# Kernel optimization log

Hardware: AMD Instinct MI355X
Metric: run time of the kernel (lower is better)

## Reference

```python
import jax, jax.numpy as jnp
import numpy as np
import math

B, T, C = 2, 2048, 1024
N_HEADS = 16  # config.head_size in the original (actually number of heads)
HEAD_DIM = C // N_HEADS


def setup_inputs() -> dict:
    key = jax.random.key(0)
    k1, k2, k3 = jax.random.split(key, 3)
    s = 1.0 / math.sqrt(C)
    return {
        "x": jax.random.normal(k1, (B, T, C), dtype=jnp.float32),
        "W_attn": jax.random.normal(k2, (C, 3 * C), dtype=jnp.float32) * s,
        "b_attn": jnp.zeros((3 * C,), dtype=jnp.float32),
        "W_proj": jax.random.normal(k3, (C, C), dtype=jnp.float32) * s,
        "b_proj": jnp.zeros((C,), dtype=jnp.float32),
    }


def reference(x, W_attn, b_attn, W_proj, b_proj):
    Bsz, Tlen, Cdim = x.shape
    qkv = x @ W_attn + b_attn                      # [B,T,3C]
    q, k, v = jnp.split(qkv, 3, axis=-1)
    # [B,T,C] -> [B,H,T,D]
    def to_heads(t):
        return t.reshape(Bsz, Tlen, N_HEADS, HEAD_DIM).transpose(0, 2, 1, 3)
    q, k, v = to_heads(q), to_heads(k), to_heads(v)
    # NOTE: original multiplies by sqrt(head_dim) (faithful to source, not 1/sqrt)
    scale = jnp.asarray(math.sqrt(HEAD_DIM), dtype=x.dtype)
    att = jnp.einsum("bhqd,bhkd->bhqk", q, k) * scale
    causal = jnp.tril(jnp.ones((Tlen, Tlen), dtype=bool))
    att = jnp.where(causal[None, None, :, :], att, jnp.asarray(-jnp.inf, x.dtype))
    att = jax.nn.softmax(att, axis=-1)
    # dropout layers are identity in eval mode
    y = jnp.einsum("bhqk,bhkd->bhqd", att, v)
    y = y.transpose(0, 2, 1, 3).reshape(Bsz, Tlen, Cdim)
    return y @ W_proj + b_proj
```

## Files before the change

### kernel.cpp

```cpp
#include <hip/hip_runtime.h>
#include <hip/hip_bf16.h>


#define B_  2
#define T_  2048
#define C_  1024
#define H_  16
#define D_  64
#define M_  (B_ * T_)
#define N3_ (3 * C_)

typedef __attribute__((ext_vector_type(8))) short s16x8;
typedef __attribute__((ext_vector_type(4))) short s16x4;
typedef __attribute__((ext_vector_type(4))) float f32x4;

typedef const __attribute__((address_space(1))) unsigned int gu32_t;
typedef __attribute__((address_space(3))) unsigned int lu32_t;

__device__ __forceinline__ void gload_lds16(const short* g, short* l) {
    __builtin_amdgcn_global_load_lds((gu32_t*)g, (lu32_t*)l, 16, 0, 0);
}

__device__ __forceinline__ float b2f(unsigned short u) {
    return __uint_as_float(((unsigned)u) << 16);
}
__device__ __forceinline__ unsigned short f2b(float f) {
    unsigned u = __float_as_uint(f);
    return (unsigned short)((u + 0x7FFFu + ((u >> 16) & 1u)) >> 16);
}

__global__ __launch_bounds__(256) void cvt_split(
    const float* __restrict__ in, short* __restrict__ oh, short* __restrict__ ol, int n)
{
    int i = (blockIdx.x * 256 + threadIdx.x) * 8;
    if (i >= n) return;
    float4 a = *(const float4*)&in[i];
    float4 b = *(const float4*)&in[i + 4];
    float v[8] = {a.x, a.y, a.z, a.w, b.x, b.y, b.z, b.w};
    s16x8 h, l;
    #pragma unroll
    for (int j = 0; j < 8; j++) {
        unsigned short hb = f2b(v[j]);
        h[j] = (short)hb;
        l[j] = (short)f2b(v[j] - b2f(hb));
    }
    *(s16x8*)&oh[i] = h;
    *(s16x8*)&ol[i] = l;
}

__global__ __launch_bounds__(256) void cvtT_split(
    const float* __restrict__ in, short* __restrict__ oh, short* __restrict__ ol,
    int R, int Cn)
{
    __shared__ short th[64][80];
    __shared__ short tl[64][80];
    const int tid = threadIdx.x;
    const int k0 = blockIdx.y * 64;
    const int n0 = blockIdx.x * 64;
    {
        int rl = tid >> 4, cl = (tid & 15) * 4;
        #pragma unroll
        for (int i = 0; i < 4; i++) {
            int kr = rl + i * 16;
            float4 v4 = *(const float4*)&in[(size_t)(k0 + kr) * Cn + n0 + cl];
            float v[4] = {v4.x, v4.y, v4.z, v4.w};
            #pragma unroll
            for (int j = 0; j < 4; j++) {
                unsigned short hb = f2b(v[j]);
                th[cl + j][kr] = (short)hb;
                tl[cl + j][kr] = (short)f2b(v[j] - b2f(hb));
            }
        }
    }
    __syncthreads();
    {
        int ro = tid >> 2, co = (tid & 3) * 16;
        *(s16x8*)&oh[(size_t)(n0 + ro) * R + k0 + co]     = *(s16x8*)&th[ro][co];
        *(s16x8*)&oh[(size_t)(n0 + ro) * R + k0 + co + 8] = *(s16x8*)&th[ro][co + 8];
        *(s16x8*)&ol[(size_t)(n0 + ro) * R + k0 + co]     = *(s16x8*)&tl[ro][co];
        *(s16x8*)&ol[(size_t)(n0 + ro) * R + k0 + co + 8] = *(s16x8*)&tl[ro][co + 8];
    }
}

__global__ __launch_bounds__(256) void cvtT_bf16(
    const float* __restrict__ in, short* __restrict__ out, int R, int Cn)
{
    __shared__ short t[64][80];
    const int tid = threadIdx.x;
    const int k0 = blockIdx.y * 64;
    const int n0 = blockIdx.x * 64;
    {
        int rl = tid >> 4, cl = (tid & 15) * 4;
        #pragma unroll
        for (int i = 0; i < 4; i++) {
            int kr = rl + i * 16;
            float4 v = *(const float4*)&in[(size_t)(k0 + kr) * Cn + n0 + cl];
            t[cl + 0][kr] = (short)f2b(v.x);
            t[cl + 1][kr] = (short)f2b(v.y);
            t[cl + 2][kr] = (short)f2b(v.z);
            t[cl + 3][kr] = (short)f2b(v.w);
        }
    }
    __syncthreads();
    {
        int ro = tid >> 2, co = (tid & 3) * 16;
        *(s16x8*)&out[(size_t)(n0 + ro) * R + k0 + co]     = *(s16x8*)&t[ro][co];
        *(s16x8*)&out[(size_t)(n0 + ro) * R + k0 + co + 8] = *(s16x8*)&t[ro][co + 8];
    }
}

__global__ __launch_bounds__(256) void qkv_qk(
    const short* __restrict__ Ah, const short* __restrict__ Al,
    const short* __restrict__ BTh, const short* __restrict__ BTl,
    const float* __restrict__ bias,
    short* __restrict__ Qh, short* __restrict__ Ql,
    short* __restrict__ Kh, short* __restrict__ Kl)
{
    __shared__ short Ash[128 * 32], Asl[128 * 32];
    __shared__ short Bsh[128 * 32], Bsl[128 * 32];

    const int tid  = threadIdx.x;
    const int wave = tid >> 6, lane = tid & 63;
    const int wm = wave >> 1, wn = wave & 1;
    const int lm = lane & 15, lq = lane >> 4;
    const int m0 = blockIdx.y * 128, n0 = blockIdx.x * 128;
    const int gr = (lane >> 2);
    const int gc = (lane & 3) * 8;

    f32x4 acc[4][4] = {};

    for (int k0 = 0; k0 < C_; k0 += 32) {
        __syncthreads();
        #pragma unroll
        for (int j = 0; j < 2; j++) {
            int s = wave * 2 + j;
            int row = s * 16 + gr;
            size_t ga = (size_t)(m0 + row) * C_ + k0 + gc;
            size_t gb = (size_t)(n0 + row) * C_ + k0 + gc;
            gload_lds16(&Ah[ga],  &Ash[s * 512]);
            gload_lds16(&Al[ga],  &Asl[s * 512]);
            gload_lds16(&BTh[gb], &Bsh[s * 512]);
            gload_lds16(&BTl[gb], &Bsl[s * 512]);
        }
        __syncthreads();

        s16x8 ah[4], al[4], bh[4], bl[4];
        #pragma unroll
        for (int mi = 0; mi < 4; mi++) {
            int r = wm * 64 + mi * 16 + lm;
            ah[mi] = *(const s16x8*)&Ash[r * 32 + lq * 8];
            al[mi] = *(const s16x8*)&Asl[r * 32 + lq * 8];
        }
        #pragma unroll
        for (int nj = 0; nj < 4; nj++) {
            int r = wn * 64 + nj * 16 + lm;
            bh[nj] = *(const s16x8*)&Bsh[r * 32 + lq * 8];
            bl[nj] = *(const s16x8*)&Bsl[r * 32 + lq * 8];
        }
        #pragma unroll
        for (int mi = 0; mi < 4; mi++)
            #pragma unroll
            for (int nj = 0; nj < 4; nj++) {
                acc[mi][nj] = __builtin_amdgcn_mfma_f32_16x16x32_bf16(
                    ah[mi], bh[nj], acc[mi][nj], 0, 0, 0);
                acc[mi][nj] = __builtin_amdgcn_mfma_f32_16x16x32_bf16(
                    ah[mi], bl[nj], acc[mi][nj], 0, 0, 0);
                acc[mi][nj] = __builtin_amdgcn_mfma_f32_16x16x32_bf16(
                    al[mi], bh[nj], acc[mi][nj], 0, 0, 0);
            }
    }

    #pragma unroll
    for (int nj = 0; nj < 4; nj++) {
        int n = n0 + wn * 64 + nj * 16 + lm;
        float bv = bias[n];
        int isK = n >> 10;
        int c = n & (C_ - 1);
        int h = c >> 6, d = c & (D_ - 1);
        short* dh = isK ? Kh : Qh;
        short* dl = isK ? Kl : Ql;
        #pragma unroll
        for (int mi = 0; mi < 4; mi++) {
            #pragma unroll
            for (int r = 0; r < 4; r++) {
                int m  = m0 + wm * 64 + mi * 16 + lq * 4 + r;
                int bb = m >> 11, t = m & (T_ - 1);
                float v = acc[mi][nj][r] + bv;
                size_t idx = (((size_t)bb * H_ + h) * T_ + t) * D_ + d;
                unsigned short hb = f2b(v);
                dh[idx] = (short)hb;
                dl[idx] = (short)f2b(v - b2f(hb));
            }
        }
    }
}

__global__ __launch_bounds__(256) void qkv_v(
    const short* __restrict__ Ah, const short* __restrict__ BTh,
    const float* __restrict__ bias, short* __restrict__ VT)
{
    __shared__ short Ash[128 * 32];
    __shared__ short Bsh[128 * 32];

    const int tid  = threadIdx.x;
    const int wave = tid >> 6, lane = tid & 63;
    const int wm = wave >> 1, wn = wave & 1;
    const int lm = lane & 15, lq = lane >> 4;
    const int m0 = blockIdx.y * 128, n0 = blockIdx.x * 128;
    const int gr = (lane >> 2);
    const int gc = (lane & 3) * 8;

    f32x4 acc[4][4] = {};

    for (int k0 = 0; k0 < C_; k0 += 32) {
        __syncthreads();
        #pragma unroll
        for (int j = 0; j < 2; j++) {
            int s = wave * 2 + j;
            int row = s * 16 + gr;
            gload_lds16(&Ah[(size_t)(m0 + row) * C_ + k0 + gc],  &Ash[s * 512]);
            gload_lds16(&BTh[(size_t)(n0 + row) * C_ + k0 + gc], &Bsh[s * 512]);
        }
        __syncthreads();

        s16x8 af[4], bfr[4];
        #pragma unroll
        for (int mi = 0; mi < 4; mi++)
            af[mi] = *(const s16x8*)&Ash[(wm * 64 + mi * 16 + lm) * 32 + lq * 8];
        #pragma unroll
        for (int nj = 0; nj < 4; nj++)
            bfr[nj] = *(const s16x8*)&Bsh[(wn * 64 + nj * 16 + lm) * 32 + lq * 8];
        #pragma unroll
        for (int mi = 0; mi < 4; mi++)
            #pragma unroll
            for (int nj = 0; nj < 4; nj++)
                acc[mi][nj] = __builtin_amdgcn_mfma_f32_16x16x32_bf16(
                    af[mi], bfr[nj], acc[mi][nj], 0, 0, 0);
    }

    #pragma unroll
    for (int nj = 0; nj < 4; nj++) {
        int n = n0 + wn * 64 + nj * 16 + lm;
        float bv = bias[n];
        int h = n >> 6, d = n & (D_ - 1);
        #pragma unroll
        for (int mi = 0; mi < 4; mi++) {
            #pragma unroll
            for (int r = 0; r < 4; r++) {
                int m  = m0 + wm * 64 + mi * 16 + lq * 4 + r;
                int bb = m >> 11, t = m & (T_ - 1);
                VT[(((size_t)bb * H_ + h) * D_ + d) * T_ + t] =
                    (short)f2b(acc[mi][nj][r] + bv);
            }
        }
    }
}

__global__ __launch_bounds__(256) void proj_mfma(
    const short* __restrict__ A, const short* __restrict__ BT,
    const float* __restrict__ bias, float* __restrict__ out)
{
    __shared__ short Ash[128 * 32];
    __shared__ short Bsh[128 * 32];

    const int tid  = threadIdx.x;
    const int wave = tid >> 6, lane = tid & 63;
    const int wm = wave >> 1, wn = wave & 1;
    const int lm = lane & 15, lq = lane >> 4;
    const int m0 = blockIdx.y * 128, n0 = blockIdx.x * 128;
    const int gr = (lane >> 2);
    const int gc = (lane & 3) * 8;

    f32x4 acc[4][4] = {};

    for (int k0 = 0; k0 < C_; k0 += 32) {
        __syncthreads();
        #pragma unroll
        for (int j = 0; j < 2; j++) {
            int s = wave * 2 + j;
            int row = s * 16 + gr;
            gload_lds16(&A[(size_t)(m0 + row) * C_ + k0 + gc],  &Ash[s * 512]);
            gload_lds16(&BT[(size_t)(n0 + row) * C_ + k0 + gc], &Bsh[s * 512]);
        }
        __syncthreads();

        s16x8 af[4], bfr[4];
        #pragma unroll
        for (int mi = 0; mi < 4; mi++)
            af[mi] = *(const s16x8*)&Ash[(wm * 64 + mi * 16 + lm) * 32 + lq * 8];
        #pragma unroll
        for (int nj = 0; nj < 4; nj++)
            bfr[nj] = *(const s16x8*)&Bsh[(wn * 64 + nj * 16 + lm) * 32 + lq * 8];
        #pragma unroll
        for (int mi = 0; mi < 4; mi++)
            #pragma unroll
            for (int nj = 0; nj < 4; nj++)
                acc[mi][nj] = __builtin_amdgcn_mfma_f32_16x16x32_bf16(
                    af[mi], bfr[nj], acc[mi][nj], 0, 0, 0);
    }

    #pragma unroll
    for (int nj = 0; nj < 4; nj++) {
        int n = n0 + wn * 64 + nj * 16 + lm;
        float bv = bias[n];
        #pragma unroll
        for (int mi = 0; mi < 4; mi++) {
            #pragma unroll
            for (int r = 0; r < 4; r++) {
                int m = m0 + wm * 64 + mi * 16 + lq * 4 + r;
                out[(size_t)m * C_ + n] = acc[mi][nj][r] + bv;
            }
        }
    }
}

__global__ __launch_bounds__(256) void attn_mfma(
    const short* __restrict__ Qh, const short* __restrict__ Ql,
    const short* __restrict__ Kh, const short* __restrict__ Kl,
    const short* __restrict__ VT, short* __restrict__ Yb)
{
    __shared__ short Qsh[64][72], Qsl[64][72];
    __shared__ short Ksh[64][72], Ksl[64][72];
    __shared__ short Vt [64][72];
    __shared__ short Ps [4][16][72];

    const int tid  = threadIdx.x;
    const int wave = tid >> 6, lane = tid & 63;
    const int lm   = lane & 15, quad = lane >> 4;
    const int bh   = blockIdx.y;
    const int b    = bh >> 4, h = bh & (H_ - 1);
    const size_t base = (size_t)bh * T_ * D_;
    const size_t vbase = (size_t)bh * D_ * T_;

    for (int half = 0; half < 2; half++) {
        const int qt = (half == 0) ? blockIdx.x : 31 - blockIdx.x;
        const int q0 = qt * 64;

        __syncthreads();
        #pragma unroll
        for (int i = 0; i < 2; i++) {
            int c = i * 256 + tid;
            int row = c >> 3, ch = (c & 7) * 8;
            size_t g = base + (size_t)(q0 + row) * D_ + ch;
            *(s16x8*)&Qsh[row][ch] = *(const s16x8*)&Qh[g];
            *(s16x8*)&Qsl[row][ch] = *(const s16x8*)&Ql[g];
        }
        __syncthreads();

        s16x8 bqh[2], bql[2];
        #pragma unroll
        for (int kc = 0; kc < 2; kc++) {
            bqh[kc] = *(const s16x8*)&Qsh[wave * 16 + lm][kc * 32 + quad * 8];
            bql[kc] = *(const s16x8*)&Qsl[wave * 16 + lm][kc * 32 + quad * 8];
        }

        float mrow = -INFINITY, lrow = 0.f;
        f32x4 O[4] = {};

        for (int kt = 0; kt <= qt; kt++) {
            __syncthreads();
            #pragma unroll
            for (int i = 0; i < 2; i++) {
                int c = i * 256 + tid;
                int row = c >> 3, ch = (c & 7) * 8;
                size_t g = base + (size_t)(kt * 64 + row) * D_ + ch;
                *(s16x8*)&Ksh[row][ch] = *(const s16x8*)&Kh[g];
                *(s16x8*)&Ksl[row][ch] = *(const s16x8*)&Kl[g];
            }
            #pragma unroll
            for (int i = 0; i < 2; i++) {
                int c = i * 256 + tid;
                int d = c >> 3, ch = (c & 7) * 8;
                *(s16x8*)&Vt[d][ch] =
                    *(const s16x8*)&VT[vbase + (size_t)d * T_ + kt * 64 + ch];
            }
            __syncthreads();

            f32x4 S[4] = {};
            #pragma unroll
            for (int t = 0; t < 4; t++) {
                #pragma unroll
                for (int kc = 0; kc < 2; kc++) {
                    s16x8 kh8 = *(const s16x8*)&Ksh[t * 16 + lm][kc * 32 + quad * 8];
                    s16x8 kl8 = *(const s16x8*)&Ksl[t * 16 + lm][kc * 32 + quad * 8];
                    S[t] = __builtin_amdgcn_mfma_f32_16x16x32_bf16(kh8, bqh[kc], S[t], 0, 0, 0);
                    S[t] = __builtin_amdgcn_mfma_f32_16x16x32_bf16(kl8, bqh[kc], S[t], 0, 0, 0);
                    S[t] = __builtin_amdgcn_mfma_f32_16x16x32_bf16(kh8, bql[kc], S[t], 0, 0, 0);
                }
            }

            const int qg = wave * 16 + lm;
            #pragma unroll
            for (int t = 0; t < 4; t++)
                #pragma unroll
                for (int r = 0; r < 4; r++) {
                    float v = S[t][r] * 8.0f;
                    if (kt == qt && (t * 16 + quad * 4 + r) > qg) v = -INFINITY;
                    S[t][r] = v;
                }

            float rm = -INFINITY;
            #pragma unroll
            for (int t = 0; t < 4; t++)
                #pragma unroll
                for (int r = 0; r < 4; r++) rm = fmaxf(rm, S[t][r]);
            rm = fmaxf(rm, __shfl_xor(rm, 16, 64));
            rm = fmaxf(rm, __shfl_xor(rm, 32, 64));
            float mnew  = fmaxf(mrow, rm);
            float alpha = __expf(mrow - mnew);
            mrow = mnew;
            float rs = 0.f;
            #pragma unroll
            for (int t = 0; t < 4; t++)
                #pragma unroll
                for (int r = 0; r < 4; r++) {
                    S[t][r] = __expf(S[t][r] - mnew);
                    rs += S[t][r];
                }
            rs += __shfl_xor(rs, 16, 64);
            rs += __shfl_xor(rs, 32, 64);
            lrow = lrow * alpha + rs;

            float al[4];
            #pragma unroll
            for (int r = 0; r < 4; r++) al[r] = __shfl(alpha, quad * 4 + r, 64);
            #pragma unroll
            for (int t = 0; t < 4; t++)
                #pragma unroll
                for (int r = 0; r < 4; r++) O[t][r] *= al[r];

            #pragma unroll
            for (int t = 0; t < 4; t++) {
                s16x4 p;
                #pragma unroll
                for (int r = 0; r < 4; r++) p[r] = (short)f2b(S[t][r]);
                *(s16x4*)&Ps[wave][lm][t * 16 + quad * 4] = p;
            }

            s16x8 ap[2];
            #pragma unroll
            for (int kc = 0; kc < 2; kc++)
                ap[kc] = *(const s16x8*)&Ps[wave][lm][kc * 32 + quad * 8];
            #pragma unroll
            for (int t = 0; t < 4; t++) {
                #pragma unroll
                for (int kc = 0; kc < 2; kc++) {
                    s16x8 bv = *(const s16x8*)&Vt[t * 16 + lm][kc * 32 + quad * 8];
                    O[t] = __builtin_amdgcn_mfma_f32_16x16x32_bf16(ap[kc], bv, O[t], 0, 0, 0);
                }
            }
        }

        float li[4];
        #pragma unroll
        for (int r = 0; r < 4; r++)
            li[r] = 1.0f / __shfl(lrow, quad * 4 + r, 64);
        #pragma unroll
        for (int t = 0; t < 4; t++)
            #pragma unroll
            for (int r = 0; r < 4; r++) {
                int q = q0 + wave * 16 + quad * 4 + r;
                int d = t * 16 + lm;
                Yb[((size_t)b * T_ + q) * C_ + h * D_ + d] =
                    (short)f2b(O[t][r] * li[r]);
            }
    }
}

extern "C" void kernel_launch(void* const* d_in, const int* in_sizes, int n_in,
                              void* d_out, int out_size, void* d_ws, size_t ws_size,
                              hipStream_t stream)
{
    const float* x      = (const float*)d_in[0];
    const float* W_attn = (const float*)d_in[1];
    const float* b_attn = (const float*)d_in[2];
    const float* W_proj = (const float*)d_in[3];
    const float* b_proj = (const float*)d_in[4];
    float* out = (float*)d_out;

    char* ws = (char*)d_ws;
    const size_t MB = 1024 * 1024;
    short* Qh   = (short*)(ws);
    short* Ql   = (short*)(ws +  8 * MB);
    short* Kh   = (short*)(ws + 16 * MB);
    short* Kl   = (short*)(ws + 24 * MB);
    short* xh   = (short*)(ws + 32 * MB);
    short* xl   = (short*)(ws + 40 * MB);
    short* WaTh = (short*)(ws + 48 * MB);
    short* WaTl = (short*)(ws + 54 * MB);
    short* WpT  = (short*)(ws + 60 * MB);
    short* VT   = (short*)(ws + 40 * MB);
    short* Yb   = (short*)(ws + 32 * MB);

    cvt_split <<<dim3(M_ * C_ / 2048), 256, 0, stream>>>(x, xh, xl, M_ * C_);
    cvtT_split<<<dim3(N3_ / 64, C_ / 64), 256, 0, stream>>>(W_attn, WaTh, WaTl, C_, N3_);
    cvtT_bf16 <<<dim3(C_ / 64, C_ / 64), 256, 0, stream>>>(W_proj, WpT, C_, C_);

    qkv_qk <<<dim3(16, 32), 256, 0, stream>>>(xh, xl, WaTh, WaTl, b_attn,
                                              Qh, Ql, Kh, Kl);
    qkv_v  <<<dim3(8, 32), 256, 0, stream>>>(xh, WaTh + (size_t)2048 * C_,
                                             b_attn + 2048, VT);
    attn_mfma<<<dim3(16, 32), 256, 0, stream>>>(Qh, Ql, Kh, Kl, VT, Yb);
    proj_mfma<<<dim3(8, 32), 256, 0, stream>>>(Yb, WpT, b_proj, out);
}
```

Before: 265.3 us.

## Prefetch K/V tiles into registers, fold Q scale, remap blocks per XCD

The attention kernel now loads the next K/V tile into registers while the current tile is being computed, which overlaps global latency with MFMA work. The sqrt(D) scale is folded into Q at the QKV projection epilogue, and the causal mask is applied only on the diagonal tile. The grid is flattened and remapped so that blocks sharing a head land on the same XCD, which should improve L2 reuse. P is converted to bf16 by truncation instead of rounding, and scaling Q before the hi/lo split changes numerics slightly; together these may cost some accuracy and add register pressure.

```diff
diff --git a/kernel.cpp b/kernel.cpp
--- a/kernel.cpp
+++ b/kernel.cpp
@@ -179,13 +179,14 @@
         int h = c >> 6, d = c & (D_ - 1);
         short* dh = isK ? Kh : Qh;
         short* dl = isK ? Kl : Ql;
+        float scale = isK ? 1.0f : 8.0f;
         #pragma unroll
         for (int mi = 0; mi < 4; mi++) {
             #pragma unroll
             for (int r = 0; r < 4; r++) {
                 int m  = m0 + wm * 64 + mi * 16 + lq * 4 + r;
                 int bb = m >> 11, t = m & (T_ - 1);
-                float v = acc[mi][nj][r] + bv;
+                float v = (acc[mi][nj][r] + bv) * scale;
                 size_t idx = (((size_t)bb * H_ + h) * T_ + t) * D_ + d;
                 unsigned short hb = f2b(v);
                 dh[idx] = (short)hb;
@@ -327,23 +328,30 @@
     const int tid  = threadIdx.x;
     const int wave = tid >> 6, lane = tid & 63;
     const int lm   = lane & 15, quad = lane >> 4;
-    const int bh   = blockIdx.y;
-    const int b    = bh >> 4, h = bh & (H_ - 1);
-    const size_t base = (size_t)bh * T_ * D_;
+
+    const int bid = blockIdx.x;
+    const int xcd = bid & 7, s = bid >> 3;
+    const int bh  = xcd * 4 + (s >> 4);
+    const int qx  = s & 15;
+    const int b   = bh >> 4, h = bh & (H_ - 1);
+    const size_t base  = (size_t)bh * T_ * D_;
     const size_t vbase = (size_t)bh * D_ * T_;
 
+    s16x8 pkh[2], pkl[2], pvt[2];
+    const int src = tid >> 3;
+    const int sch = (tid & 7) * 8;
+
     for (int half = 0; half < 2; half++) {
-        const int qt = (half == 0) ? blockIdx.x : 31 - blockIdx.x;
+        const int qt = (half == 0) ? qx : 31 - qx;
         const int q0 = qt * 64;
 
         __syncthreads();
         #pragma unroll
         for (int i = 0; i < 2; i++) {
-            int c = i * 256 + tid;
-            int row = c >> 3, ch = (c & 7) * 8;
-            size_t g = base + (size_t)(q0 + row) * D_ + ch;
-            *(s16x8*)&Qsh[row][ch] = *(const s16x8*)&Qh[g];
-            *(s16x8*)&Qsl[row][ch] = *(const s16x8*)&Ql[g];
+            int row = i * 32 + src;
+            size_t g = base + (size_t)(q0 + row) * D_ + sch;
+            *(s16x8*)&Qsh[row][sch] = *(const s16x8*)&Qh[g];
+            *(s16x8*)&Qsl[row][sch] = *(const s16x8*)&Ql[g];
         }
         __syncthreads();
 
@@ -354,6 +362,15 @@
             bql[kc] = *(const s16x8*)&Qsl[wave * 16 + lm][kc * 32 + quad * 8];
         }
 
+        #pragma unroll
+        for (int i = 0; i < 2; i++) {
+            int row = i * 32 + src;
+            size_t g = base + (size_t)(row) * D_ + sch;
+            pkh[i] = *(const s16x8*)&Kh[g];
+            pkl[i] = *(const s16x8*)&Kl[g];
+            pvt[i] = *(const s16x8*)&VT[vbase + (size_t)row * T_ + sch];
+        }
+
         float mrow = -INFINITY, lrow = 0.f;
         f32x4 O[4] = {};
 
@@ -361,18 +378,20 @@
             __syncthreads();
             #pragma unroll
             for (int i = 0; i < 2; i++) {
-                int c = i * 256 + tid;
-                int row = c >> 3, ch = (c & 7) * 8;
-                size_t g = base + (size_t)(kt * 64 + row) * D_ + ch;
-                *(s16x8*)&Ksh[row][ch] = *(const s16x8*)&Kh[g];
-                *(s16x8*)&Ksl[row][ch] = *(const s16x8*)&Kl[g];
-            }
-            #pragma unroll
-            for (int i = 0; i < 2; i++) {
-                int c = i * 256 + tid;
-                int d = c >> 3, ch = (c & 7) * 8;
-                *(s16x8*)&Vt[d][ch] =
-                    *(const s16x8*)&VT[vbase + (size_t)d * T_ + kt * 64 + ch];
+                int row = i * 32 + src;
+                *(s16x8*)&Ksh[row][sch] = pkh[i];
+                *(s16x8*)&Ksl[row][sch] = pkl[i];
+                *(s16x8*)&Vt [row][sch] = pvt[i];
+            }
+            if (kt < qt) {
+                #pragma unroll
+                for (int i = 0; i < 2; i++) {
+                    int row = i * 32 + src;
+                    size_t g = base + (size_t)((kt + 1) * 64 + row) * D_ + sch;
+                    pkh[i] = *(const s16x8*)&Kh[g];
+                    pkl[i] = *(const s16x8*)&Kl[g];
+                    pvt[i] = *(const s16x8*)&VT[vbase + (size_t)row * T_ + (kt + 1) * 64 + sch];
+                }
             }
             __syncthreads();
 
@@ -390,14 +409,13 @@
             }
 
             const int qg = wave * 16 + lm;
-            #pragma unroll
-            for (int t = 0; t < 4; t++)
-                #pragma unroll
-                for (int r = 0; r < 4; r++) {
-                    float v = S[t][r] * 8.0f;
-                    if (kt == qt && (t * 16 + quad * 4 + r) > qg) v = -INFINITY;
-                    S[t][r] = v;
-                }
+            if (kt == qt) {
+                #pragma unroll
+                for (int t = 0; t < 4; t++)
+                    #pragma unroll
+                    for (int r = 0; r < 4; r++)
+                        if ((t * 16 + quad * 4 + r) > qg) S[t][r] = -INFINITY;
+            }
 
             float rm = -INFINITY;
             #pragma unroll
@@ -433,7 +451,8 @@
             for (int t = 0; t < 4; t++) {
                 s16x4 p;
                 #pragma unroll
-                for (int r = 0; r < 4; r++) p[r] = (short)f2b(S[t][r]);
+                for (int r = 0; r < 4; r++)
+                    p[r] = (short)(__float_as_uint(S[t][r]) >> 16);
                 *(s16x4*)&Ps[wave][lm][t * 16 + quad * 4] = p;
             }
 
@@ -500,6 +519,6 @@
                                               Qh, Ql, Kh, Kl);
     qkv_v  <<<dim3(8, 32), 256, 0, stream>>>(xh, WaTh + (size_t)2048 * C_,
                                              b_attn + 2048, VT);
-    attn_mfma<<<dim3(16, 32), 256, 0, stream>>>(Qh, Ql, Kh, Kl, VT, Yb);
+    attn_mfma<<<dim3(512), 256, 0, stream>>>(Qh, Ql, Kh, Kl, VT, Yb);
     proj_mfma<<<dim3(8, 32), 256, 0, stream>>>(Yb, WpT, b_proj, out);
 }
```

Measured after the change: 255.8 us. -3.6%, faster.
